# Optimization experiments

Measured on AMD Instinct MI355X. Metric: run time of the kernel, lower is better.

## Reference

```python
import jax, jax.numpy as jnp
import numpy as np

NUM_CLASSES = 10000
EMBED_DIM = 512
BATCH = 4096


def setup_inputs() -> dict:
    key = jax.random.key(0)
    k1, k2, k3 = jax.random.split(key, 3)
    x = jax.random.normal(k1, (BATCH, EMBED_DIM), dtype=jnp.float32)
    labels = jax.random.randint(k2, (BATCH,), 0, NUM_CLASSES, dtype=jnp.int64)
    centers = jax.random.normal(k3, (NUM_CLASSES, EMBED_DIM), dtype=jnp.float32)
    return {"x": x, "labels": labels, "centers": centers}


def reference(x, labels, centers):
    # distmat[b, c] = ||x_b||^2 + ||center_c||^2 - 2 <x_b, center_c>   -> (B, C)
    x_sq = jnp.sum(x * x, axis=1, keepdims=True)               # (B, 1)
    c_sq = jnp.sum(centers * centers, axis=1)[None, :]         # (1, C)
    distmat = x_sq + c_sq - 2.0 * jnp.einsum('bd,cd->bc', x, centers)
    # mask: entry where class index equals the sample's label
    mask = (labels[:, None] == jnp.arange(NUM_CLASSES)[None, :]).astype(x.dtype)
    dist = distmat * mask
    # NOTE: clamp is applied to the *masked* matrix, so the (B*C - B) zero
    # entries are clamped up to 1e-12 and included in the sum (faithful to torch).
    loss = jnp.sum(jnp.clip(dist, 1e-12, 1e12)) / x.shape[0]
    return loss
```

## Files before the change

kernel.cpp:

```cpp
#include <hip/hip_runtime.h>


#define BATCH 4096
#define DIM 512
#define NUM_CLASSES 10000
#define ROWS_PER_BLOCK 4
#define NUM_BLOCKS (BATCH / ROWS_PER_BLOCK)

__global__ __launch_bounds__(256) void center_loss_partial(
    const float* __restrict__ x,
    const int* __restrict__ labels,
    const float* __restrict__ centers,
    float* __restrict__ partials)
{
    const int wave = threadIdx.x >> 6;
    const int lane = threadIdx.x & 63;
    const int row  = blockIdx.x * ROWS_PER_BLOCK + wave;

    const int lbl = labels[row];

    const float4* xp = (const float4*)(x + (size_t)row * DIM);
    const float4* cp = (const float4*)(centers + (size_t)lbl * DIM);

    float4 a0 = xp[lane];
    float4 a1 = xp[lane + 64];
    float4 b0 = cp[lane];
    float4 b1 = cp[lane + 64];

    float d, acc = 0.0f;
    d = a0.x - b0.x; acc += d * d;
    d = a0.y - b0.y; acc += d * d;
    d = a0.z - b0.z; acc += d * d;
    d = a0.w - b0.w; acc += d * d;
    d = a1.x - b1.x; acc += d * d;
    d = a1.y - b1.y; acc += d * d;
    d = a1.z - b1.z; acc += d * d;
    d = a1.w - b1.w; acc += d * d;

    #pragma unroll
    for (int off = 32; off > 0; off >>= 1)
        acc += __shfl_down(acc, off, 64);

    __shared__ float s[ROWS_PER_BLOCK];
    if (lane == 0) {
        s[wave] = fminf(fmaxf(acc, 1e-12f), 1e12f);
    }
    __syncthreads();
    if (threadIdx.x == 0) {
        partials[blockIdx.x] = s[0] + s[1] + s[2] + s[3];
    }
}

__global__ __launch_bounds__(256) void center_loss_final(
    const float* __restrict__ partials,
    float* __restrict__ out)
{
    const int wave = threadIdx.x >> 6;
    const int lane = threadIdx.x & 63;

    float acc = 0.0f;
    for (int i = threadIdx.x; i < NUM_BLOCKS; i += 256)
        acc += partials[i];

    #pragma unroll
    for (int off = 32; off > 0; off >>= 1)
        acc += __shfl_down(acc, off, 64);

    __shared__ float s[4];
    if (lane == 0) s[wave] = acc;
    __syncthreads();
    if (threadIdx.x == 0) {
        double total = (double)s[0] + (double)s[1] + (double)s[2] + (double)s[3];
        total += (double)BATCH * (double)(NUM_CLASSES - 1) * 1e-12;
        out[0] = (float)(total / (double)BATCH);
    }
}

extern "C" void kernel_launch(void* const* d_in, const int* in_sizes, int n_in,
                              void* d_out, int out_size, void* d_ws, size_t ws_size,
                              hipStream_t stream) {
    const float* x       = (const float*)d_in[0];
    const int*   labels  = (const int*)d_in[1];
    const float* centers = (const float*)d_in[2];
    float* out = (float*)d_out;
    float* partials = (float*)d_ws;

    center_loss_partial<<<NUM_BLOCKS, 256, 0, stream>>>(x, labels, centers, partials);
    center_loss_final<<<1, 256, 0, stream>>>(partials, out);
}
```

Baseline: 74.05 us.

## Fuse partial and final reduction via atomicAdd, process four rows per wave

Merges the two-kernel reduction into a single kernel. Each block scales its partial sum and atomically adds it into the output, which a memset zeroes beforehand. Each wave now handles four rows, issuing all loads up front to raise memory-level parallelism, and the grid shrinks from 1024 to 256 blocks. This removes one kernel launch and the partials round-trip, but adds a memset call, float atomic contention, and nondeterministic summation order in fp32 instead of double.

```diff
diff --git a/kernel.cpp b/kernel.cpp
--- a/kernel.cpp
+++ b/kernel.cpp
@@ -4,75 +4,72 @@
 #define BATCH 4096
 #define DIM 512
 #define NUM_CLASSES 10000
-#define ROWS_PER_BLOCK 4
+#define ROWS_PER_WAVE 4
+#define WAVES_PER_BLOCK 4
+#define ROWS_PER_BLOCK (ROWS_PER_WAVE * WAVES_PER_BLOCK)
 #define NUM_BLOCKS (BATCH / ROWS_PER_BLOCK)
 
-__global__ __launch_bounds__(256) void center_loss_partial(
+__global__ __launch_bounds__(256) void center_loss_fused(
     const float* __restrict__ x,
     const int* __restrict__ labels,
     const float* __restrict__ centers,
-    float* __restrict__ partials)
-{
-    const int wave = threadIdx.x >> 6;
-    const int lane = threadIdx.x & 63;
-    const int row  = blockIdx.x * ROWS_PER_BLOCK + wave;
-
-    const int lbl = labels[row];
-
-    const float4* xp = (const float4*)(x + (size_t)row * DIM);
-    const float4* cp = (const float4*)(centers + (size_t)lbl * DIM);
-
-    float4 a0 = xp[lane];
-    float4 a1 = xp[lane + 64];
-    float4 b0 = cp[lane];
-    float4 b1 = cp[lane + 64];
-
-    float d, acc = 0.0f;
-    d = a0.x - b0.x; acc += d * d;
-    d = a0.y - b0.y; acc += d * d;
-    d = a0.z - b0.z; acc += d * d;
-    d = a0.w - b0.w; acc += d * d;
-    d = a1.x - b1.x; acc += d * d;
-    d = a1.y - b1.y; acc += d * d;
-    d = a1.z - b1.z; acc += d * d;
-    d = a1.w - b1.w; acc += d * d;
-
-    #pragma unroll
-    for (int off = 32; off > 0; off >>= 1)
-        acc += __shfl_down(acc, off, 64);
-
-    __shared__ float s[ROWS_PER_BLOCK];
-    if (lane == 0) {
-        s[wave] = fminf(fmaxf(acc, 1e-12f), 1e12f);
-    }
-    __syncthreads();
-    if (threadIdx.x == 0) {
-        partials[blockIdx.x] = s[0] + s[1] + s[2] + s[3];
-    }
-}
-
-__global__ __launch_bounds__(256) void center_loss_final(
-    const float* __restrict__ partials,
     float* __restrict__ out)
 {
     const int wave = threadIdx.x >> 6;
     const int lane = threadIdx.x & 63;
+    const int row0 = blockIdx.x * ROWS_PER_BLOCK + wave * ROWS_PER_WAVE;
 
-    float acc = 0.0f;
-    for (int i = threadIdx.x; i < NUM_BLOCKS; i += 256)
-        acc += partials[i];
+    float4 a[ROWS_PER_WAVE][2], b[ROWS_PER_WAVE][2];
+    #pragma unroll
+    for (int r = 0; r < ROWS_PER_WAVE; ++r) {
+        const int row = row0 + r;
+        const int lbl = labels[row];
+        const float4* xp = (const float4*)(x + (size_t)row * DIM);
+        const float4* cp = (const float4*)(centers + (size_t)lbl * DIM);
+        a[r][0] = xp[lane];
+        a[r][1] = xp[lane + 64];
+        b[r][0] = cp[lane];
+        b[r][1] = cp[lane + 64];
+    }
+
+    float acc[ROWS_PER_WAVE];
+    #pragma unroll
+    for (int r = 0; r < ROWS_PER_WAVE; ++r) {
+        float d, s = 0.0f;
+        d = a[r][0].x - b[r][0].x; s += d * d;
+        d = a[r][0].y - b[r][0].y; s += d * d;
+        d = a[r][0].z - b[r][0].z; s += d * d;
+        d = a[r][0].w - b[r][0].w; s += d * d;
+        d = a[r][1].x - b[r][1].x; s += d * d;
+        d = a[r][1].y - b[r][1].y; s += d * d;
+        d = a[r][1].z - b[r][1].z; s += d * d;
+        d = a[r][1].w - b[r][1].w; s += d * d;
+        acc[r] = s;
+    }
 
     #pragma unroll
-    for (int off = 32; off > 0; off >>= 1)
-        acc += __shfl_down(acc, off, 64);
+    for (int off = 32; off > 0; off >>= 1) {
+        #pragma unroll
+        for (int r = 0; r < ROWS_PER_WAVE; ++r)
+            acc[r] += __shfl_down(acc[r], off, 64);
+    }
 
-    __shared__ float s[4];
-    if (lane == 0) s[wave] = acc;
+    __shared__ float s_wave[WAVES_PER_BLOCK];
+    if (lane == 0) {
+        float w = 0.0f;
+        #pragma unroll
+        for (int r = 0; r < ROWS_PER_WAVE; ++r)
+            w += fminf(fmaxf(acc[r], 1e-12f), 1e12f);
+        s_wave[wave] = w;
+    }
     __syncthreads();
     if (threadIdx.x == 0) {
-        double total = (double)s[0] + (double)s[1] + (double)s[2] + (double)s[3];
-        total += (double)BATCH * (double)(NUM_CLASSES - 1) * 1e-12;
-        out[0] = (float)(total / (double)BATCH);
+        float blk = s_wave[0] + s_wave[1] + s_wave[2] + s_wave[3];
+        float v = blk * (1.0f / BATCH);
+        if (blockIdx.x == 0) {
+            v += (float)(NUM_CLASSES - 1) * 1e-12f;
+        }
+        atomicAdd(out, v);
     }
 }
 
@@ -83,8 +80,7 @@
     const int*   labels  = (const int*)d_in[1];
     const float* centers = (const float*)d_in[2];
     float* out = (float*)d_out;
-    float* partials = (float*)d_ws;
 
-    center_loss_partial<<<NUM_BLOCKS, 256, 0, stream>>>(x, labels, centers, partials);
-    center_loss_final<<<1, 256, 0, stream>>>(partials, out);
+    hipMemsetAsync(out, 0, sizeof(float), stream);
+    center_loss_fused<<<NUM_BLOCKS, 256, 0, stream>>>(x, labels, centers, out);
 }
```

Result: slower. 76.80 us (+3.7%).
